# Optimization experiments

Hardware: AMD Instinct MI355X
Metric: run time of the kernel (lower is better)

Reference implementation:

```python
import jax, jax.numpy as jnp
import numpy as np

N, D_IN, HID, NH = 16384, 2048, 2048, 16
HD = HID // NH  # head_size = 128


def setup_inputs() -> dict:
    key = jax.random.key(0)
    ks = jax.random.split(key, 8)
    s = 1.0 / np.sqrt(D_IN)
    return {
        "protein": jax.random.normal(ks[0], (N, D_IN), jnp.float32),
        "drug": jax.random.normal(ks[1], (N, D_IN), jnp.float32),
        "mask_prot": jnp.ones((N,), bool),
        "mask_drug": jnp.ones((N,), bool),
        "Wq_p": jax.random.uniform(ks[2], (D_IN, HID), jnp.float32, -s, s),
        "Wk_p": jax.random.uniform(ks[3], (D_IN, HID), jnp.float32, -s, s),
        "Wv_p": jax.random.uniform(ks[4], (D_IN, HID), jnp.float32, -s, s),
        "Wq_d": jax.random.uniform(ks[5], (D_IN, HID), jnp.float32, -s, s),
        "Wk_d": jax.random.uniform(ks[6], (D_IN, HID), jnp.float32, -s, s),
        "Wv_d": jax.random.uniform(ks[7], (D_IN, HID), jnp.float32, -s, s),
    }


def _heads(x):
    # [N, L, HID] -> [N, L, NH, HD]
    return x.reshape(x.shape[0], x.shape[1], NH, HD)


def _alpha_logits(logits, mask_row, mask_col, inf=1e6):
    # logits: [N, L1, L2, H]; masks: [N, L1], [N, L2] (broadcast over heads)
    mask_pair = mask_row[:, :, None, None] & mask_col[:, None, :, None]
    logits = jnp.where(mask_pair, logits, logits - inf)
    alpha = jax.nn.softmax(logits, axis=2)
    alpha = jnp.where(mask_row[:, :, None, None], alpha, jnp.zeros_like(alpha))
    return alpha


def reference(protein, drug, mask_prot, mask_drug, Wq_p, Wk_p, Wv_p, Wq_d, Wk_d, Wv_d):
    p = protein[:, None, :]  # [N, 1, D_IN]
    d = drug[:, None, :]
    # forward() overwrites the masks with all-ones of shape [N, L=1]
    m_p = jnp.ones(p.shape[:-1], bool)
    m_d = jnp.ones(d.shape[:-1], bool)

    qp = _heads(jnp.einsum('bld,dh->blh', p, Wq_p))  # [N,1,NH,HD]
    kp = _heads(jnp.einsum('bld,dh->blh', p, Wk_p))
    vp = _heads(jnp.einsum('bld,dh->blh', p, Wv_p))
    qd = _heads(jnp.einsum('bld,dh->blh', d, Wq_d))
    kd = _heads(jnp.einsum('bld,dh->blh', d, Wk_d))
    vd = _heads(jnp.einsum('bld,dh->blh', d, Wv_d))

    logits_pp = jnp.einsum('blhd,bkhd->blkh', qp, kp)
    logits_pd = jnp.einsum('blhd,bkhd->blkh', qp, kd)
    logits_dp = jnp.einsum('blhd,bkhd->blkh', qd, kp)
    logits_dd = jnp.einsum('blhd,bkhd->blkh', qd, kd)

    a_pp = _alpha_logits(logits_pp, m_p, m_p)
    a_pd = _alpha_logits(logits_pd, m_p, m_d)
    a_dp = _alpha_logits(logits_dp, m_d, m_p)
    a_dd = _alpha_logits(logits_dd, m_d, m_d)

    def agg(alpha, v):
        out = jnp.einsum('blkh,bkhd->blhd', alpha, v)
        return out.reshape(out.shape[0], out.shape[1], HID)

    prot_embedding = (agg(a_pp, vp) + agg(a_pd, vd)) / 2  # [N,1,HID]
    drug_embedding = (agg(a_dp, vp) + agg(a_dd, vd)) / 2

    # agg_mode == 'cls'
    prot_embed = prot_embedding[:, 0]
    drug_embed = drug_embedding[:, 0]
    return jnp.concatenate([prot_embed, drug_embed], axis=1)  # [N, 2*HID]
```

## Files before the change

kernel.cpp:

```cpp
#include <hip/hip_runtime.h>
#include <stdint.h>


typedef __attribute__((ext_vector_type(8))) short short8;
typedef __attribute__((ext_vector_type(4))) float float4v;
typedef __attribute__((ext_vector_type(2))) unsigned int uint2v;

typedef const __attribute__((address_space(1))) unsigned int* gp_t;
typedef __attribute__((address_space(3))) unsigned int* lp_t;

#define M_DIM 16384
#define N_DIM 2048
#define K_DIM 4096
#define OUT_LD 4096

static __device__ __forceinline__ unsigned int pack_bf16x2(float x, float y) {
  union { float f; unsigned int u; } a, b;
  a.f = x; b.f = y;
  unsigned int ua = a.u + 0x8000u;
  unsigned int ub = b.u + 0x8000u;
  return __builtin_amdgcn_perm(ub, ua, 0x07060302u);
}

static __device__ __forceinline__ unsigned short f2bf(float x) {
  union { float f; unsigned int u; } a; a.f = x;
  return (unsigned short)((a.u + 0x8000u) >> 16);
}

__global__ __launch_bounds__(256)
void prep_wt(const float* __restrict__ Wp, const float* __restrict__ Wd,
             unsigned short* __restrict__ Wt) {
  __shared__ float tile[32][33];
  const int k0 = blockIdx.x * 32;
  const int n0 = blockIdx.y * 32;
  const int tx = threadIdx.x;
  const int ty = threadIdx.y;
  const float* W = (k0 < 2048) ? Wp : Wd;
  const int kk0 = (k0 < 2048) ? k0 : k0 - 2048;
#pragma unroll
  for (int i = 0; i < 4; ++i) {
    int r = ty * 4 + i;
    tile[r][tx] = W[(size_t)(kk0 + r) * 2048 + n0 + tx];
  }
  __syncthreads();
#pragma unroll
  for (int i = 0; i < 4; ++i) {
    int r = ty * 4 + i;
    Wt[(size_t)(n0 + r) * (size_t)K_DIM + k0 + tx] = f2bf(tile[tx][r]);
  }
}

__global__ __launch_bounds__(256)
void cast_a(const float* __restrict__ P, const float* __restrict__ Dg,
            unsigned int* __restrict__ Abf) {
  int idx = blockIdx.x * 256 + threadIdx.x;
  int row = idx >> 10;
  int j = (idx & 1023) << 2;
  const float* src = (j < 2048) ? (P + (size_t)row * 2048 + j)
                                : (Dg + (size_t)row * 2048 + (j - 2048));
  float4v v = *(const float4v*)src;
  uint2v o;
  o.x = pack_bf16x2(v.x, v.y);
  o.y = pack_bf16x2(v.z, v.w);
  *(uint2v*)(Abf + (size_t)row * 2048 + (j >> 1)) = o;
}


#define VMW(N) asm volatile("s_waitcnt vmcnt(" #N ")" ::: "memory")
#define LGW0() asm volatile("s_waitcnt lgkmcnt(0)" ::: "memory")
#define BAR() __builtin_amdgcn_s_barrier()

#define LOAD_A(Ac, QM)                                                      \
  _Pragma("unroll") for (int i = 0; i < 4; ++i) {                           \
    af[i][0] = *(const short8*)&(Ac)[aoff + ((QM)*4 + i) * 1024 + c0];      \
    af[i][1] = *(const short8*)&(Ac)[aoff + ((QM)*4 + i) * 1024 + c1];      \
  }

#define LOAD_B2(dst, Bc, QN)                                                \
  _Pragma("unroll") for (int j = 0; j < 2; ++j) {                           \
    dst[j][0] = *(const short8*)&(Bc)[boff + ((QN)*2 + j) * 1024 + c0];     \
    dst[j][1] = *(const short8*)&(Bc)[boff + ((QN)*2 + j) * 1024 + c1];     \
  }

#define MFMA_Q(bset, QM, QN)                                                \
  _Pragma("unroll") for (int i = 0; i < 4; ++i)                             \
  _Pragma("unroll") for (int j = 0; j < 2; ++j) {                           \
    acc[(QM)*4 + i][(QN)*2 + j] = __builtin_amdgcn_mfma_f32_16x16x32_bf16(  \
        af[i][0], bset[j][0], acc[(QM)*4 + i][(QN)*2 + j], 0, 0, 0);        \
    acc[(QM)*4 + i][(QN)*2 + j] = __builtin_amdgcn_mfma_f32_16x16x32_bf16(  \
        af[i][1], bset[j][1], acc[(QM)*4 + i][(QN)*2 + j], 0, 0, 0);        \
  }

__global__ __launch_bounds__(512, 2)
void gemm8(const unsigned short* __restrict__ Abf,
           const unsigned short* __restrict__ Wt,
           float* __restrict__ out) {
  __shared__ unsigned short As[2][256 * 64];
  __shared__ unsigned short Bs[2][256 * 64];

  const int t = threadIdx.x;
  const int w = t >> 6, l = t & 63;
  const int wm = w >> 2, wn = w & 3;
  const int lr = l & 15, q16 = l >> 4, xr = lr & 7;

  const int bx = blockIdx.x;
  const int logical = (bx & 7) * 64 + (bx >> 3);
  const int tn = logical & 7, tm = logical >> 3;
  const int m0 = tm << 8, n0 = tn << 8;

  const int srow = t >> 3;
  const int sk = (((t & 7) ^ (srow & 7)) << 3);
  const int brr = srow & 31;
  const int bsel = t >> 8;

  auto stage_a = [&](int buf, int k0, int h) {
#pragma unroll
    for (int sub = 0; sub < 2; ++sub) {
      const int row = m0 + sub * 128 + h * 64 + srow;
      const unsigned short* g = Abf + (size_t)row * K_DIM + (k0 + sk);
      const int ldsrow0 = sub * 128 + h * 64 + (w << 3);
      __builtin_amdgcn_global_load_lds((gp_t)(const void*)g,
                                       (lp_t)&As[buf][ldsrow0 * 64], 16, 0, 0);
    }
  };
  auto stage_b = [&](int buf, int k0, int nh) {
#pragma unroll
    for (int sub = 0; sub < 2; ++sub) {
      const int wnr = sub * 2 + bsel;
      const int ncol = n0 + wnr * 64 + nh * 32 + brr;
      const unsigned short* g = Wt + (size_t)ncol * K_DIM + (k0 + sk);
      const int ldsrow0 = wnr * 64 + nh * 32 + ((w & 3) << 3);
      __builtin_amdgcn_global_load_lds((gp_t)(const void*)g,
                                       (lp_t)&Bs[buf][ldsrow0 * 64], 16, 0, 0);
    }
  };

  float4v acc[8][4];
#pragma unroll
  for (int i = 0; i < 8; ++i)
#pragma unroll
    for (int j = 0; j < 4; ++j)
      acc[i][j] = (float4v){0.f, 0.f, 0.f, 0.f};

  const int aoff = (wm * 128 + lr) * 64;
  const int boff = (wn * 64 + lr) * 64;
  const int c0 = (q16 ^ xr) << 3;
  const int c1 = ((4 + q16) ^ xr) << 3;

  stage_a(0, 0, 0);
  stage_b(0, 0, 0);
  stage_b(0, 0, 1);
  stage_a(0, 0, 1);
  stage_a(1, 64, 0);
  stage_b(1, 64, 0);
  stage_b(1, 64, 1);
  stage_a(1, 64, 1);
  VMW(8);
  BAR();

  for (int tt = 0; tt < 62; ++tt) {
    const int buf = tt & 1;
    unsigned short* Ac = &As[buf][0];
    unsigned short* Bc = &Bs[buf][0];
    const int k2 = tt * 64 + 128;
    short8 af[4][2];
    short8 b0r[2][2];
    short8 b1r[2][2];

    LOAD_A(Ac, 0)
    LOAD_B2(b0r, Bc, 0)
    BAR(); LGW0();
    __builtin_amdgcn_s_setprio(1);
    MFMA_Q(b0r, 0, 0)
    __builtin_amdgcn_s_setprio(0);
    BAR();

    LOAD_B2(b1r, Bc, 1)
    stage_a(buf, k2, 0);
    stage_b(buf, k2, 0);
    BAR(); LGW0();
    __builtin_amdgcn_s_setprio(1);
    MFMA_Q(b1r, 0, 1)
    __builtin_amdgcn_s_setprio(0);
    BAR();

    LOAD_A(Ac, 1)
    stage_b(buf, k2, 1);
    BAR(); LGW0();
    __builtin_amdgcn_s_setprio(1);
    MFMA_Q(b1r, 1, 1)
    __builtin_amdgcn_s_setprio(0);
    BAR();

    stage_a(buf, k2, 1);
    BAR();
    __builtin_amdgcn_s_setprio(1);
    MFMA_Q(b0r, 1, 0)
    __builtin_amdgcn_s_setprio(0);
    VMW(8);
    BAR();
  }

  VMW(0);
  BAR();
#pragma unroll
  for (int e = 0; e < 2; ++e) {
    unsigned short* Ac = &As[e][0];
    unsigned short* Bc = &Bs[e][0];
    short8 af[4][2];
    short8 b0r[2][2];
    short8 b1r[2][2];
    __builtin_amdgcn_s_setprio(1);
    LOAD_A(Ac, 0)
    LOAD_B2(b0r, Bc, 0)
    MFMA_Q(b0r, 0, 0)
    LOAD_B2(b1r, Bc, 1)
    MFMA_Q(b1r, 0, 1)
    LOAD_A(Ac, 1)
    MFMA_Q(b1r, 1, 1)
    MFMA_Q(b0r, 1, 0)
    __builtin_amdgcn_s_setprio(0);
  }

  const int rbase = m0 + wm * 128 + q16 * 4;
  const int cbase = n0 + wn * 64 + lr;
#pragma unroll
  for (int f = 0; f < 8; ++f)
#pragma unroll
    for (int j = 0; j < 4; ++j) {
      const int row = rbase + f * 16;
      const int col = cbase + j * 16;
#pragma unroll
      for (int r = 0; r < 4; ++r) {
        float v = acc[f][j][r] * 0.5f;
        size_t o = (size_t)(row + r) * (size_t)OUT_LD + col;
        out[o] = v;
        out[o + N_DIM] = v;
      }
    }
}

__global__ __launch_bounds__(256)
void gemm_k(const float* __restrict__ Ap, const float* __restrict__ Ad,
            const unsigned short* __restrict__ Wt,
            float* __restrict__ out) {
  __shared__ unsigned short As[128 * 64];
  __shared__ unsigned short Bsm[128 * 64];

  const int t = threadIdx.x;
  const int bx = blockIdx.x;
  const int tn = bx & 15, tm = bx >> 4;
  const int m0 = tm << 7, n0 = tn << 7;
  const int w = t >> 6, l = t & 63;
  const int wmm = w & 1, wnn = w >> 1;
  const int lr = l & 15, q = l >> 4;

  const int rB = t >> 3;
  const int kB = (t & 7) * 8;

  float4v acc[4][4];
#pragma unroll
  for (int i = 0; i < 4; ++i)
#pragma unroll
    for (int j = 0; j < 4; ++j)
      acc[i][j] = (float4v){0.f, 0.f, 0.f, 0.f};

  for (int k0 = 0; k0 < K_DIM; k0 += 64) {
#pragma unroll
    for (int i = 0; i < 4; ++i) {
      const unsigned short* g =
          Wt + (size_t)(n0 + i * 32 + rB) * (size_t)K_DIM + (k0 + kB);
      __builtin_amdgcn_global_load_lds((gp_t)(const void*)g,
                                       (lp_t)&Bsm[i * 2048 + w * 512], 16, 0, 0);
    }
    {
      const float* base;
      int kk;
      if (k0 < 2048) { base = Ap; kk = k0; } else { base = Ad; kk = k0 - 2048; }
      const int rA = t >> 4;
      const int cA = (t & 15) * 4;
#pragma unroll
      for (int i = 0; i < 8; ++i) {
        int m = i * 16 + rA;
        float4v v = *(const float4v*)(base + (size_t)(m0 + m) * 2048 + kk + cA);
        uint2v o;
        o.x = pack_bf16x2(v.x, v.y);
        o.y = pack_bf16x2(v.z, v.w);
        *(uint2v*)&As[m * 64 + cA] = o;
      }
    }
    __syncthreads();

#pragma unroll
    for (int ks = 0; ks < 2; ++ks) {
      short8 a2[4], b2[4];
#pragma unroll
      for (int i = 0; i < 4; ++i) {
        a2[i] = *(const short8*)&As[(wmm * 64 + i * 16 + lr) * 64 + ks * 32 + q * 8];
        b2[i] = *(const short8*)&Bsm[(wnn * 64 + i * 16 + lr) * 64 + ks * 32 + q * 8];
      }
#pragma unroll
      for (int i = 0; i < 4; ++i)
#pragma unroll
        for (int j = 0; j < 4; ++j)
          acc[i][j] = __builtin_amdgcn_mfma_f32_16x16x32_bf16(a2[i], b2[j],
                                                              acc[i][j], 0, 0, 0);
    }
    __syncthreads();
  }

#pragma unroll
  for (int i = 0; i < 4; ++i) {
    const int r0 = m0 + wmm * 64 + i * 16 + q * 4;
#pragma unroll
    for (int j = 0; j < 4; ++j) {
      const int c = n0 + wnn * 64 + j * 16 + lr;
#pragma unroll
      for (int r = 0; r < 4; ++r) {
        float v = acc[i][j][r] * 0.5f;
        size_t o = (size_t)(r0 + r) * (size_t)OUT_LD + c;
        out[o] = v;
        out[o + 2048] = v;
      }
    }
  }
}

__global__ __launch_bounds__(256)
void gemm_fallback(const float* __restrict__ P, const float* __restrict__ Dg,
                   const float* __restrict__ Wp, const float* __restrict__ Wd,
                   float* __restrict__ out) {
  __shared__ float Asf[64][17];
  __shared__ float Bsf[16][65];
  const int bx = blockIdx.x;
  const int by = blockIdx.y;
  const int t = threadIdx.x;
  const int tc = t & 15, trw = t >> 4;
  const int m0 = by * 64, n0 = bx * 64;
  float accf[4][4] = {};
  for (int k0 = 0; k0 < 4096; k0 += 16) {
    const float* Asrc = (k0 < 2048) ? P : Dg;
    const float* Bsrc = (k0 < 2048) ? Wp : Wd;
    const int kk = k0 & 2047;
#pragma unroll
    for (int i = 0; i < 4; ++i) {
      int r = i * 16 + trw;
      Asf[r][tc] = Asrc[(size_t)(m0 + r) * 2048 + kk + tc];
    }
#pragma unroll
    for (int i = 0; i < 4; ++i) {
      int r = i * 4 + (t >> 6);
      int c = t & 63;
      Bsf[r][c] = Bsrc[(size_t)(kk + r) * 2048 + n0 + c];
    }
    __syncthreads();
#pragma unroll
    for (int k2 = 0; k2 < 16; ++k2) {
      float a[4], b[4];
#pragma unroll
      for (int i = 0; i < 4; ++i) a[i] = Asf[trw * 4 + i][k2];
#pragma unroll
      for (int j = 0; j < 4; ++j) b[j] = Bsf[k2][tc * 4 + j];
#pragma unroll
      for (int i = 0; i < 4; ++i)
#pragma unroll
        for (int j = 0; j < 4; ++j) accf[i][j] += a[i] * b[j];
    }
    __syncthreads();
  }
#pragma unroll
  for (int i = 0; i < 4; ++i)
#pragma unroll
    for (int j = 0; j < 4; ++j) {
      float v = accf[i][j] * 0.5f;
      size_t o = (size_t)(m0 + trw * 4 + i) * 4096 + n0 + tc * 4 + j;
      out[o] = v;
      out[o + 2048] = v;
    }
}

extern "C" void kernel_launch(void* const* d_in, const int* in_sizes, int n_in,
                              void* d_out, int out_size, void* d_ws, size_t ws_size,
                              hipStream_t stream) {
  const float* protein = (const float*)d_in[0];
  const float* drug    = (const float*)d_in[1];
  const float* Wv_p    = (const float*)d_in[6];
  const float* Wv_d    = (const float*)d_in[9];
  float* out = (float*)d_out;

  const size_t wt_bytes = (size_t)N_DIM * K_DIM * sizeof(unsigned short);
  const size_t a_bytes  = (size_t)M_DIM * K_DIM * sizeof(unsigned short);

  if (ws_size >= wt_bytes) {
    unsigned short* Wt = (unsigned short*)d_ws;
    prep_wt<<<dim3(128, 64), dim3(32, 8), 0, stream>>>(Wv_p, Wv_d, Wt);
    if (ws_size >= wt_bytes + a_bytes) {
      unsigned int* Abf = (unsigned int*)((char*)d_ws + wt_bytes);
      cast_a<<<65536, 256, 0, stream>>>(protein, drug, Abf);
      gemm8<<<512, 512, 0, stream>>>((const unsigned short*)Abf, Wt, out);
    } else {
      gemm_k<<<2048, 256, 0, stream>>>(protein, drug, Wt, out);
    }
  } else {
    gemm_fallback<<<dim3(32, 256), 256, 0, stream>>>(protein, drug, Wv_p, Wv_d, out);
  }
}
```

Baseline: 825.8 us.

## Restructure GEMM main loop into register double-buffered K-half MFMA phases

Reorganizes the bf16 GEMM main loop so each phase computes a 4x4 MFMA block over one 32-wide K half, with ping-pong A/B register fragments. The next tile's first fragments are loaded from the other LDS buffer during the current iteration, hiding LDS latency behind MFMAs. Global-to-LDS staging is rescheduled: the second A half is staged into the alternate buffer one tile ahead, with adjusted vmcnt waits. Sched barriers pin instruction order, and the epilogue is rewritten to match. The risk is subtle LDS hazards from the new staging order and higher register pressure under launch bounds of 512 threads x 2.

```diff
diff --git a/kernel.cpp b/kernel.cpp
--- a/kernel.cpp
+++ b/kernel.cpp
@@ -69,27 +69,24 @@
 #define VMW(N) asm volatile("s_waitcnt vmcnt(" #N ")" ::: "memory")
 #define LGW0() asm volatile("s_waitcnt lgkmcnt(0)" ::: "memory")
 #define BAR() __builtin_amdgcn_s_barrier()
-
-#define LOAD_A(Ac, QM)                                                      \
-  _Pragma("unroll") for (int i = 0; i < 4; ++i) {                           \
-    af[i][0] = *(const short8*)&(Ac)[aoff + ((QM)*4 + i) * 1024 + c0];      \
-    af[i][1] = *(const short8*)&(Ac)[aoff + ((QM)*4 + i) * 1024 + c1];      \
-  }
-
-#define LOAD_B2(dst, Bc, QN)                                                \
-  _Pragma("unroll") for (int j = 0; j < 2; ++j) {                           \
-    dst[j][0] = *(const short8*)&(Bc)[boff + ((QN)*2 + j) * 1024 + c0];     \
-    dst[j][1] = *(const short8*)&(Bc)[boff + ((QN)*2 + j) * 1024 + c1];     \
-  }
-
-#define MFMA_Q(bset, QM, QN)                                                \
+#define SBAR0() __builtin_amdgcn_sched_barrier(0)
+#define SP1 __builtin_amdgcn_s_setprio(1);
+#define SP0 __builtin_amdgcn_s_setprio(0);
+
+#define LOAD_A4(dst, base, H, KS)                                           \
   _Pragma("unroll") for (int i = 0; i < 4; ++i)                             \
-  _Pragma("unroll") for (int j = 0; j < 2; ++j) {                           \
-    acc[(QM)*4 + i][(QN)*2 + j] = __builtin_amdgcn_mfma_f32_16x16x32_bf16(  \
-        af[i][0], bset[j][0], acc[(QM)*4 + i][(QN)*2 + j], 0, 0, 0);        \
-    acc[(QM)*4 + i][(QN)*2 + j] = __builtin_amdgcn_mfma_f32_16x16x32_bf16(  \
-        af[i][1], bset[j][1], acc[(QM)*4 + i][(QN)*2 + j], 0, 0, 0);        \
-  }
+    dst[i] = *(const short8*)&(base)[aoff + ((H)*4 + i) * 1024 +            \
+                                     ((KS) ? c1 : c0)];
+
+#define LOAD_B4(dst, base, KS)                                              \
+  _Pragma("unroll") for (int j = 0; j < 4; ++j)                             \
+    dst[j] = *(const short8*)&(base)[boff + j * 1024 + ((KS) ? c1 : c0)];
+
+#define MFMA16(ASET, BSET, MB)                                              \
+  _Pragma("unroll") for (int i = 0; i < 4; ++i)                             \
+  _Pragma("unroll") for (int j = 0; j < 4; ++j)                             \
+    acc[(MB) + i][j] = __builtin_amdgcn_mfma_f32_16x16x32_bf16(             \
+        ASET[i], BSET[j], acc[(MB) + i][j], 0, 0, 0);
 
 __global__ __launch_bounds__(512, 2)
 void gemm8(const unsigned short* __restrict__ Abf,
@@ -147,79 +144,92 @@
   const int c0 = (q16 ^ xr) << 3;
   const int c1 = ((4 + q16) ^ xr) << 3;
 
+  short8 aA[4], aB[4], bA[4], bB[4];
+
   stage_a(0, 0, 0);
+  stage_a(0, 0, 1);
   stage_b(0, 0, 0);
   stage_b(0, 0, 1);
-  stage_a(0, 0, 1);
   stage_a(1, 64, 0);
   stage_b(1, 64, 0);
   stage_b(1, 64, 1);
-  stage_a(1, 64, 1);
-  VMW(8);
+  VMW(6);
   BAR();
+  {
+    unsigned short* Ac = &As[0][0];
+    unsigned short* Bc = &Bs[0][0];
+    LOAD_A4(aA, Ac, 0, 0)
+    LOAD_B4(bA, Bc, 0)
+  }
 
   for (int tt = 0; tt < 62; ++tt) {
     const int buf = tt & 1;
     unsigned short* Ac = &As[buf][0];
     unsigned short* Bc = &Bs[buf][0];
+    unsigned short* An = &As[buf ^ 1][0];
+    unsigned short* Bn = &Bs[buf ^ 1][0];
+    const int k1 = tt * 64 + 64;
     const int k2 = tt * 64 + 128;
-    short8 af[4][2];
-    short8 b0r[2][2];
-    short8 b1r[2][2];
-
-    LOAD_A(Ac, 0)
-    LOAD_B2(b0r, Bc, 0)
-    BAR(); LGW0();
-    __builtin_amdgcn_s_setprio(1);
-    MFMA_Q(b0r, 0, 0)
-    __builtin_amdgcn_s_setprio(0);
-    BAR();
-
-    LOAD_B2(b1r, Bc, 1)
+
+    BAR(); LGW0();
+    stage_a(buf ^ 1, k1, 1);
+    LOAD_A4(aB, Ac, 1, 0)
+    SBAR0(); SP1 MFMA16(aA, bA, 0) SP0
+
+    BAR(); LGW0();
+    LOAD_B4(bB, Bc, 1)
+    LOAD_A4(aA, Ac, 0, 1)
+    SBAR0(); SP1 MFMA16(aB, bA, 4) SP0
+
+    BAR(); VMW(2); LGW0();
+    LOAD_A4(aB, Ac, 1, 1)
+    SBAR0(); SP1 MFMA16(aA, bB, 0) SP0
+
+    BAR(); LGW0();
     stage_a(buf, k2, 0);
     stage_b(buf, k2, 0);
-    BAR(); LGW0();
-    __builtin_amdgcn_s_setprio(1);
-    MFMA_Q(b1r, 0, 1)
-    __builtin_amdgcn_s_setprio(0);
-    BAR();
-
-    LOAD_A(Ac, 1)
     stage_b(buf, k2, 1);
-    BAR(); LGW0();
-    __builtin_amdgcn_s_setprio(1);
-    MFMA_Q(b1r, 1, 1)
-    __builtin_amdgcn_s_setprio(0);
-    BAR();
-
-    stage_a(buf, k2, 1);
-    BAR();
-    __builtin_amdgcn_s_setprio(1);
-    MFMA_Q(b0r, 1, 0)
-    __builtin_amdgcn_s_setprio(0);
-    VMW(8);
-    BAR();
-  }
-
-  VMW(0);
-  BAR();
-#pragma unroll
-  for (int e = 0; e < 2; ++e) {
-    unsigned short* Ac = &As[e][0];
-    unsigned short* Bc = &Bs[e][0];
-    short8 af[4][2];
-    short8 b0r[2][2];
-    short8 b1r[2][2];
-    __builtin_amdgcn_s_setprio(1);
-    LOAD_A(Ac, 0)
-    LOAD_B2(b0r, Bc, 0)
-    MFMA_Q(b0r, 0, 0)
-    LOAD_B2(b1r, Bc, 1)
-    MFMA_Q(b1r, 0, 1)
-    LOAD_A(Ac, 1)
-    MFMA_Q(b1r, 1, 1)
-    MFMA_Q(b0r, 1, 0)
-    __builtin_amdgcn_s_setprio(0);
+    LOAD_A4(aA, An, 0, 0)
+    LOAD_B4(bA, Bn, 0)
+    SBAR0(); SP1 MFMA16(aB, bB, 4) SP0
+    VMW(6);
+  }
+
+  {
+    unsigned short* Ac0 = &As[0][0];
+    unsigned short* Bc0 = &Bs[0][0];
+    unsigned short* Ac1 = &As[1][0];
+    unsigned short* Bc1 = &Bs[1][0];
+
+    BAR(); LGW0();
+    stage_a(1, 4032, 1);
+    LOAD_A4(aB, Ac0, 1, 0)
+    SBAR0(); SP1 MFMA16(aA, bA, 0) SP0
+    BAR(); LGW0();
+    LOAD_B4(bB, Bc0, 1)
+    LOAD_A4(aA, Ac0, 0, 1)
+    SBAR0(); SP1 MFMA16(aB, bA, 4) SP0
+    BAR(); LGW0();
+    LOAD_A4(aB, Ac0, 1, 1)
+    SBAR0(); SP1 MFMA16(aA, bB, 0) SP0
+    VMW(0);
+    BAR(); LGW0();
+    LOAD_A4(aA, Ac1, 0, 0)
+    LOAD_B4(bA, Bc1, 0)
+    SBAR0(); SP1 MFMA16(aB, bB, 4) SP0
+
+    LGW0();
+    LOAD_A4(aB, Ac1, 1, 0)
+    SBAR0(); SP1 MFMA16(aA, bA, 0) SP0
+    LGW0();
+    LOAD_B4(bB, Bc1, 1)
+    LOAD_A4(aA, Ac1, 0, 1)
+    SBAR0(); SP1 MFMA16(aB, bA, 4) SP0
+    LGW0();
+    LOAD_A4(aB, Ac1, 1, 1)
+    SBAR0(); SP1 MFMA16(aA, bB, 0) SP0
+    LGW0();
+    SBAR0(); SP1 MFMA16(aB, bB, 4) SP0
   }
 
   const int rbase = m0 + wm * 128 + q16 * 4;
```

After: 867.2 us. 1.05x slower.

## Fuse fp32-to-bf16 activation cast into GEMM mainloop with register-staged prefetch

Applied to the files above, without the earlier changes.

Removes the separate cast_a kernel and its bf16 workspace round trip. The GEMM now loads fp32 activations straight into registers, packs them to bf16 and writes them into swizzled LDS, with one half-tile prefetched ahead and interleaved between the MFMA phases. This saves a full extra write and read of the activation matrix, but it doubles the A-side global bytes the GEMM reads and raises register pressure. It also replaces the asynchronous global-to-LDS loads with synchronous VGPR staging, which may expose latency.

```diff
diff --git a/kernel.cpp b/kernel.cpp
--- a/kernel.cpp
+++ b/kernel.cpp
@@ -50,25 +50,12 @@
   }
 }
 
-__global__ __launch_bounds__(256)
-void cast_a(const float* __restrict__ P, const float* __restrict__ Dg,
-            unsigned int* __restrict__ Abf) {
-  int idx = blockIdx.x * 256 + threadIdx.x;
-  int row = idx >> 10;
-  int j = (idx & 1023) << 2;
-  const float* src = (j < 2048) ? (P + (size_t)row * 2048 + j)
-                                : (Dg + (size_t)row * 2048 + (j - 2048));
-  float4v v = *(const float4v*)src;
-  uint2v o;
-  o.x = pack_bf16x2(v.x, v.y);
-  o.y = pack_bf16x2(v.z, v.w);
-  *(uint2v*)(Abf + (size_t)row * 2048 + (j >> 1)) = o;
-}
-
 
 #define VMW(N) asm volatile("s_waitcnt vmcnt(" #N ")" ::: "memory")
 #define LGW0() asm volatile("s_waitcnt lgkmcnt(0)" ::: "memory")
 #define BAR() __builtin_amdgcn_s_barrier()
+#define SP1 __builtin_amdgcn_s_setprio(1);
+#define SP0 __builtin_amdgcn_s_setprio(0);
 
 #define LOAD_A(Ac, QM)                                                      \
   _Pragma("unroll") for (int i = 0; i < 4; ++i) {                           \
@@ -92,7 +79,7 @@
   }
 
 __global__ __launch_bounds__(512, 2)
-void gemm8(const unsigned short* __restrict__ Abf,
+void gemm8(const float* __restrict__ Pp, const float* __restrict__ Dd,
            const unsigned short* __restrict__ Wt,
            float* __restrict__ out) {
   __shared__ unsigned short As[2][256 * 64];
@@ -113,16 +100,6 @@
   const int brr = srow & 31;
   const int bsel = t >> 8;
 
-  auto stage_a = [&](int buf, int k0, int h) {
-#pragma unroll
-    for (int sub = 0; sub < 2; ++sub) {
-      const int row = m0 + sub * 128 + h * 64 + srow;
-      const unsigned short* g = Abf + (size_t)row * K_DIM + (k0 + sk);
-      const int ldsrow0 = sub * 128 + h * 64 + (w << 3);
-      __builtin_amdgcn_global_load_lds((gp_t)(const void*)g,
-                                       (lp_t)&As[buf][ldsrow0 * 64], 16, 0, 0);
-    }
-  };
   auto stage_b = [&](int buf, int k0, int nh) {
 #pragma unroll
     for (int sub = 0; sub < 2; ++sub) {
@@ -135,6 +112,32 @@
     }
   };
 
+  const int s_r = t >> 4;
+  const int s_c = (t & 15) * 4;
+
+  auto loadA = [&](float4v* v, int h, int k0) {
+    const float* base; int kk;
+    if (k0 < 2048) { base = Pp; kk = k0; } else { base = Dd; kk = k0 - 2048; }
+#pragma unroll
+    for (int s = 0; s < 4; ++s) {
+      const int rh = s * 32 + s_r;
+      const int row = m0 + (rh >> 6) * 128 + h * 64 + (rh & 63);
+      v[s] = *(const float4v*)(base + (size_t)row * 2048 + kk + s_c);
+    }
+  };
+  auto writeA = [&](int buf, int h, const float4v* v) {
+#pragma unroll
+    for (int s = 0; s < 4; ++s) {
+      const int rh = s * 32 + s_r;
+      const int row_lds = (rh >> 6) * 128 + h * 64 + (rh & 63);
+      const int col_sw = (((s_c >> 3) ^ (rh & 7)) << 3) + (s_c & 7);
+      uint2v u;
+      u.x = pack_bf16x2(v[s].x, v[s].y);
+      u.y = pack_bf16x2(v[s].z, v[s].w);
+      *(uint2v*)&As[buf][row_lds * 64 + col_sw] = u;
+    }
+  };
+
   float4v acc[8][4];
 #pragma unroll
   for (int i = 0; i < 8; ++i)
@@ -147,70 +150,72 @@
   const int c0 = (q16 ^ xr) << 3;
   const int c1 = ((4 + q16) ^ xr) << 3;
 
-  stage_a(0, 0, 0);
+  float4v vA0[4], vA1[4];
+
+  {
+    float4v vT[4];
+#pragma unroll
+    for (int q = 0; q < 2; ++q)
+#pragma unroll
+      for (int h = 0; h < 2; ++h) {
+        loadA(vT, h, q * 64);
+        writeA(q, h, vT);
+      }
+  }
   stage_b(0, 0, 0);
   stage_b(0, 0, 1);
-  stage_a(0, 0, 1);
-  stage_a(1, 64, 0);
   stage_b(1, 64, 0);
   stage_b(1, 64, 1);
-  stage_a(1, 64, 1);
-  VMW(8);
+  loadA(vA0, 0, 128);
+  VMW(4);
+  LGW0();
   BAR();
 
+  short8 af[4][2];
+  short8 b0r[2][2];
+  short8 b1r[2][2];
   for (int tt = 0; tt < 62; ++tt) {
     const int buf = tt & 1;
     unsigned short* Ac = &As[buf][0];
     unsigned short* Bc = &Bs[buf][0];
     const int k2 = tt * 64 + 128;
-    short8 af[4][2];
-    short8 b0r[2][2];
-    short8 b1r[2][2];
+    const int k3 = (tt < 61) ? tt * 64 + 192 : 0;
 
     LOAD_A(Ac, 0)
     LOAD_B2(b0r, Bc, 0)
     BAR(); LGW0();
-    __builtin_amdgcn_s_setprio(1);
-    MFMA_Q(b0r, 0, 0)
-    __builtin_amdgcn_s_setprio(0);
+    SP1 MFMA_Q(b0r, 0, 0) SP0
     BAR();
 
     LOAD_B2(b1r, Bc, 1)
-    stage_a(buf, k2, 0);
+    loadA(vA1, 1, k2);
+    writeA(buf, 0, vA0);
     stage_b(buf, k2, 0);
     BAR(); LGW0();
-    __builtin_amdgcn_s_setprio(1);
-    MFMA_Q(b1r, 0, 1)
-    __builtin_amdgcn_s_setprio(0);
+    SP1 MFMA_Q(b1r, 0, 1) SP0
     BAR();
 
     LOAD_A(Ac, 1)
     stage_b(buf, k2, 1);
     BAR(); LGW0();
-    __builtin_amdgcn_s_setprio(1);
-    MFMA_Q(b1r, 1, 1)
-    __builtin_amdgcn_s_setprio(0);
+    SP1 MFMA_Q(b1r, 1, 1) SP0
     BAR();
 
-    stage_a(buf, k2, 1);
+    writeA(buf, 1, vA1);
+    loadA(vA0, 0, k3);
+    BAR(); LGW0();
+    SP1 MFMA_Q(b0r, 1, 0) SP0
     BAR();
-    __builtin_amdgcn_s_setprio(1);
-    MFMA_Q(b0r, 1, 0)
-    __builtin_amdgcn_s_setprio(0);
-    VMW(8);
-    BAR();
   }
 
   VMW(0);
+  LGW0();
   BAR();
 #pragma unroll
   for (int e = 0; e < 2; ++e) {
     unsigned short* Ac = &As[e][0];
     unsigned short* Bc = &Bs[e][0];
-    short8 af[4][2];
-    short8 b0r[2][2];
-    short8 b1r[2][2];
-    __builtin_amdgcn_s_setprio(1);
+    SP1
     LOAD_A(Ac, 0)
     LOAD_B2(b0r, Bc, 0)
     MFMA_Q(b0r, 0, 0)
@@ -219,7 +224,7 @@
     LOAD_A(Ac, 1)
     MFMA_Q(b1r, 1, 1)
     MFMA_Q(b0r, 1, 0)
-    __builtin_amdgcn_s_setprio(0);
+    SP0
   }
 
   const int rbase = m0 + wm * 128 + q16 * 4;
@@ -238,92 +243,6 @@
         out[o + N_DIM] = v;
       }
     }
-}
-
-__global__ __launch_bounds__(256)
-void gemm_k(const float* __restrict__ Ap, const float* __restrict__ Ad,
-            const unsigned short* __restrict__ Wt,
-            float* __restrict__ out) {
-  __shared__ unsigned short As[128 * 64];
-  __shared__ unsigned short Bsm[128 * 64];
-
-  const int t = threadIdx.x;
-  const int bx = blockIdx.x;
-  const int tn = bx & 15, tm = bx >> 4;
-  const int m0 = tm << 7, n0 = tn << 7;
-  const int w = t >> 6, l = t & 63;
-  const int wmm = w & 1, wnn = w >> 1;
-  const int lr = l & 15, q = l >> 4;
-
-  const int rB = t >> 3;
-  const int kB = (t & 7) * 8;
-
-  float4v acc[4][4];
-#pragma unroll
-  for (int i = 0; i < 4; ++i)
-#pragma unroll
-    for (int j = 0; j < 4; ++j)
-      acc[i][j] = (float4v){0.f, 0.f, 0.f, 0.f};
-
-  for (int k0 = 0; k0 < K_DIM; k0 += 64) {
-#pragma unroll
-    for (int i = 0; i < 4; ++i) {
-      const unsigned short* g =
-          Wt + (size_t)(n0 + i * 32 + rB) * (size_t)K_DIM + (k0 + kB);
-      __builtin_amdgcn_global_load_lds((gp_t)(const void*)g,
-                                       (lp_t)&Bsm[i * 2048 + w * 512], 16, 0, 0);
-    }
-    {
-      const float* base;
-      int kk;
-      if (k0 < 2048) { base = Ap; kk = k0; } else { base = Ad; kk = k0 - 2048; }
-      const int rA = t >> 4;
-      const int cA = (t & 15) * 4;
-#pragma unroll
-      for (int i = 0; i < 8; ++i) {
-        int m = i * 16 + rA;
-        float4v v = *(const float4v*)(base + (size_t)(m0 + m) * 2048 + kk + cA);
-        uint2v o;
-        o.x = pack_bf16x2(v.x, v.y);
-        o.y = pack_bf16x2(v.z, v.w);
-        *(uint2v*)&As[m * 64 + cA] = o;
-      }
-    }
-    __syncthreads();
-
-#pragma unroll
-    for (int ks = 0; ks < 2; ++ks) {
-      short8 a2[4], b2[4];
-#pragma unroll
-      for (int i = 0; i < 4; ++i) {
-        a2[i] = *(const short8*)&As[(wmm * 64 + i * 16 + lr) * 64 + ks * 32 + q * 8];
-        b2[i] = *(const short8*)&Bsm[(wnn * 64 + i * 16 + lr) * 64 + ks * 32 + q * 8];
-      }
-#pragma unroll
-      for (int i = 0; i < 4; ++i)
-#pragma unroll
-        for (int j = 0; j < 4; ++j)
-          acc[i][j] = __builtin_amdgcn_mfma_f32_16x16x32_bf16(a2[i], b2[j],
-                                                              acc[i][j], 0, 0, 0);
-    }
-    __syncthreads();
-  }
-
-#pragma unroll
-  for (int i = 0; i < 4; ++i) {
-    const int r0 = m0 + wmm * 64 + i * 16 + q * 4;
-#pragma unroll
-    for (int j = 0; j < 4; ++j) {
-      const int c = n0 + wnn * 64 + j * 16 + lr;
-#pragma unroll
-      for (int r = 0; r < 4; ++r) {
-        float v = acc[i][j][r] * 0.5f;
-        size_t o = (size_t)(r0 + r) * (size_t)OUT_LD + c;
-        out[o] = v;
-        out[o + 2048] = v;
-      }
-    }
-  }
 }
 
 __global__ __launch_bounds__(256)
@@ -389,18 +308,11 @@
   float* out = (float*)d_out;
 
   const size_t wt_bytes = (size_t)N_DIM * K_DIM * sizeof(unsigned short);
-  const size_t a_bytes  = (size_t)M_DIM * K_DIM * sizeof(unsigned short);
 
   if (ws_size >= wt_bytes) {
     unsigned short* Wt = (unsigned short*)d_ws;
     prep_wt<<<dim3(128, 64), dim3(32, 8), 0, stream>>>(Wv_p, Wv_d, Wt);
-    if (ws_size >= wt_bytes + a_bytes) {
-      unsigned int* Abf = (unsigned int*)((char*)d_ws + wt_bytes);
-      cast_a<<<65536, 256, 0, stream>>>(protein, drug, Abf);
-      gemm8<<<512, 512, 0, stream>>>((const unsigned short*)Abf, Wt, out);
-    } else {
-      gemm_k<<<2048, 256, 0, stream>>>(protein, drug, Wt, out);
-    }
+    gemm8<<<512, 512, 0, stream>>>(protein, drug, Wt, out);
   } else {
     gemm_fallback<<<dim3(32, 256), 256, 0, stream>>>(protein, drug, Wv_p, Wv_d, out);
   }
```

Result: slower. 948.2 us (+14.8%).

## Restructure GEMM main loop to register-prefetch full tile and single barrier per step

Applied to the files above, without the earlier changes.

Replaces the four-phase per-iteration schedule, which had several barriers and partial LDS fragment loads, with one schedule per K-step. All A and B fragments for the tile are held in registers, and the next tile's LDS reads are interleaved with the current MFMAs. Global-to-LDS staging for the following tile is issued up front, with a single full vmcnt/lgkmcnt wait and one barrier per iteration. Launch bounds move from 2 to 1 blocks per CU to make room for the extra registers, which costs occupancy. The full vmcnt(0) wait each iteration may also expose global load latency.

```diff
diff --git a/kernel.cpp b/kernel.cpp
--- a/kernel.cpp
+++ b/kernel.cpp
@@ -69,29 +69,10 @@
 #define VMW(N) asm volatile("s_waitcnt vmcnt(" #N ")" ::: "memory")
 #define LGW0() asm volatile("s_waitcnt lgkmcnt(0)" ::: "memory")
 #define BAR() __builtin_amdgcn_s_barrier()
-
-#define LOAD_A(Ac, QM)                                                      \
-  _Pragma("unroll") for (int i = 0; i < 4; ++i) {                           \
-    af[i][0] = *(const short8*)&(Ac)[aoff + ((QM)*4 + i) * 1024 + c0];      \
-    af[i][1] = *(const short8*)&(Ac)[aoff + ((QM)*4 + i) * 1024 + c1];      \
-  }
-
-#define LOAD_B2(dst, Bc, QN)                                                \
-  _Pragma("unroll") for (int j = 0; j < 2; ++j) {                           \
-    dst[j][0] = *(const short8*)&(Bc)[boff + ((QN)*2 + j) * 1024 + c0];     \
-    dst[j][1] = *(const short8*)&(Bc)[boff + ((QN)*2 + j) * 1024 + c1];     \
-  }
-
-#define MFMA_Q(bset, QM, QN)                                                \
-  _Pragma("unroll") for (int i = 0; i < 4; ++i)                             \
-  _Pragma("unroll") for (int j = 0; j < 2; ++j) {                           \
-    acc[(QM)*4 + i][(QN)*2 + j] = __builtin_amdgcn_mfma_f32_16x16x32_bf16(  \
-        af[i][0], bset[j][0], acc[(QM)*4 + i][(QN)*2 + j], 0, 0, 0);        \
-    acc[(QM)*4 + i][(QN)*2 + j] = __builtin_amdgcn_mfma_f32_16x16x32_bf16(  \
-        af[i][1], bset[j][1], acc[(QM)*4 + i][(QN)*2 + j], 0, 0, 0);        \
-  }
-
-__global__ __launch_bounds__(512, 2)
+#define SP1 __builtin_amdgcn_s_setprio(1);
+#define SP0 __builtin_amdgcn_s_setprio(0);
+
+__global__ __launch_bounds__(512, 1)
 void gemm8(const unsigned short* __restrict__ Abf,
            const unsigned short* __restrict__ Wt,
            float* __restrict__ out) {
@@ -147,80 +128,75 @@
   const int c0 = (q16 ^ xr) << 3;
   const int c1 = ((4 + q16) ^ xr) << 3;
 
+  short8 aR[8][2];
+  short8 bR[4][2];
+
   stage_a(0, 0, 0);
+  stage_a(0, 0, 1);
   stage_b(0, 0, 0);
   stage_b(0, 0, 1);
-  stage_a(0, 0, 1);
   stage_a(1, 64, 0);
   stage_b(1, 64, 0);
   stage_b(1, 64, 1);
   stage_a(1, 64, 1);
   VMW(8);
   BAR();
+  {
+    const unsigned short* Ac = &As[0][0];
+    const unsigned short* Bc = &Bs[0][0];
+#pragma unroll
+    for (int i = 0; i < 8; ++i) {
+      aR[i][0] = *(const short8*)&Ac[aoff + i * 1024 + c0];
+      aR[i][1] = *(const short8*)&Ac[aoff + i * 1024 + c1];
+    }
+#pragma unroll
+    for (int j = 0; j < 4; ++j) {
+      bR[j][0] = *(const short8*)&Bc[boff + j * 1024 + c0];
+      bR[j][1] = *(const short8*)&Bc[boff + j * 1024 + c1];
+    }
+  }
+  LGW0();
+  BAR();
+
+  auto tile_mfma = [&](const unsigned short* AcN, const unsigned short* BcN,
+                       bool doread) {
+    SP1
+#pragma unroll
+    for (int ks = 0; ks < 2; ++ks) {
+      const int cks = ks ? c1 : c0;
+#pragma unroll
+      for (int i = 0; i < 8; ++i) {
+#pragma unroll
+        for (int j = 0; j < 4; ++j)
+          acc[i][j] = __builtin_amdgcn_mfma_f32_16x16x32_bf16(
+              aR[i][ks], bR[j][ks], acc[i][j], 0, 0, 0);
+        if (doread)
+          aR[i][ks] = *(const short8*)&AcN[aoff + i * 1024 + cks];
+      }
+      if (doread) {
+#pragma unroll
+        for (int j = 0; j < 4; ++j)
+          bR[j][ks] = *(const short8*)&BcN[boff + j * 1024 + cks];
+      }
+    }
+    SP0
+  };
 
   for (int tt = 0; tt < 62; ++tt) {
     const int buf = tt & 1;
-    unsigned short* Ac = &As[buf][0];
-    unsigned short* Bc = &Bs[buf][0];
     const int k2 = tt * 64 + 128;
-    short8 af[4][2];
-    short8 b0r[2][2];
-    short8 b1r[2][2];
-
-    LOAD_A(Ac, 0)
-    LOAD_B2(b0r, Bc, 0)
-    BAR(); LGW0();
-    __builtin_amdgcn_s_setprio(1);
-    MFMA_Q(b0r, 0, 0)
-    __builtin_amdgcn_s_setprio(0);
+    stage_a(buf, k2, 0);
+    stage_a(buf, k2, 1);
+    stage_b(buf, k2, 0);
+    stage_b(buf, k2, 1);
+    tile_mfma(&As[buf ^ 1][0], &Bs[buf ^ 1][0], true);
+    VMW(0);
+    LGW0();
     BAR();
-
-    LOAD_B2(b1r, Bc, 1)
-    stage_a(buf, k2, 0);
-    stage_b(buf, k2, 0);
-    BAR(); LGW0();
-    __builtin_amdgcn_s_setprio(1);
-    MFMA_Q(b1r, 0, 1)
-    __builtin_amdgcn_s_setprio(0);
-    BAR();
-
-    LOAD_A(Ac, 1)
-    stage_b(buf, k2, 1);
-    BAR(); LGW0();
-    __builtin_amdgcn_s_setprio(1);
-    MFMA_Q(b1r, 1, 1)
-    __builtin_amdgcn_s_setprio(0);
-    BAR();
-
-    stage_a(buf, k2, 1);
-    BAR();
-    __builtin_amdgcn_s_setprio(1);
-    MFMA_Q(b0r, 1, 0)
-    __builtin_amdgcn_s_setprio(0);
-    VMW(8);
-    BAR();
-  }
-
-  VMW(0);
-  BAR();
-#pragma unroll
-  for (int e = 0; e < 2; ++e) {
-    unsigned short* Ac = &As[e][0];
-    unsigned short* Bc = &Bs[e][0];
-    short8 af[4][2];
-    short8 b0r[2][2];
-    short8 b1r[2][2];
-    __builtin_amdgcn_s_setprio(1);
-    LOAD_A(Ac, 0)
-    LOAD_B2(b0r, Bc, 0)
-    MFMA_Q(b0r, 0, 0)
-    LOAD_B2(b1r, Bc, 1)
-    MFMA_Q(b1r, 0, 1)
-    LOAD_A(Ac, 1)
-    MFMA_Q(b1r, 1, 1)
-    MFMA_Q(b0r, 1, 0)
-    __builtin_amdgcn_s_setprio(0);
-  }
+  }
+
+  tile_mfma(&As[1][0], &Bs[1][0], true);
+  tile_mfma(nullptr, nullptr, false);
 
   const int rbase = m0 + wm * 128 + q16 * 4;
   const int cbase = n0 + wn * 64 + lr;
```

Result: faster. 754.6 us (-8.6%).
